# Performance work log

Measured on AMD Instinct MI355X. Metric: run time of the kernel, lower is better.

The kernel has to match this reference:

```python
import jax, jax.numpy as jnp
import numpy as np

B, N, FIN, H, F = 8, 1024, 256, 8, 64
NEG_SLOPE = 0.2


def setup_inputs() -> dict:
    key = jax.random.key(0)
    k = jax.random.split(key, 6)
    x = jax.random.normal(k[0], (B, N, FIN), dtype=jnp.float32)
    adj_mask = jax.random.randint(k[1], (B, N, N), 0, 2, dtype=jnp.int32)
    edge_prior = jax.random.normal(k[2], (B, N, N), dtype=jnp.float32)
    # params (xavier-style scales)
    W = jax.random.normal(k[3], (FIN, H * F), dtype=jnp.float32) * np.sqrt(2.0 / (FIN + H * F))
    a_left = jax.random.normal(k[4], (H, F), dtype=jnp.float32) * np.sqrt(2.0 / (1 + F))
    a_right = jax.random.normal(k[5], (H, F), dtype=jnp.float32) * np.sqrt(2.0 / (1 + F))
    edge_scale = jnp.float32(0.05)
    return {"x": x, "adj_mask": adj_mask, "edge_prior": edge_prior,
            "W": W, "a_left": a_left, "a_right": a_right, "edge_scale": edge_scale}


def reference(x, adj_mask, edge_prior, W, a_left, a_right, edge_scale):
    b, n, _ = x.shape
    h = (x @ W).reshape(b, n, H, F)                      # [B,N,H,F]
    e_left = jnp.einsum('bnhf,hf->bnh', h, a_left)       # [B,N,H]
    e_right = jnp.einsum('bnhf,hf->bnh', h, a_right)     # [B,N,H]
    e = jax.nn.leaky_relu(e_left[:, :, None, :] + e_right[:, None, :, :],
                          negative_slope=NEG_SLOPE)      # [B,N,N,H]
    e = e + edge_scale * edge_prior[..., None]
    e = jnp.where((adj_mask == 0)[..., None], -jnp.inf, e)
    alpha = jax.nn.softmax(e, axis=2)                    # softmax over neighbors j
    h_new = jnp.einsum('bijh,bjhf->bihf', alpha, h)      # [B,N,H,F]
    return h_new.reshape(b, n, H * F)                    # concat=True
```

## Files before the change

### kernel.cpp

```cpp
#include <hip/hip_runtime.h>
#include <hip/hip_bf16.h>

#define B_ 8
#define N_ 1024
#define FIN_ 256
#define H_ 8
#define F_ 64
#define HF_ 512
#define BN_ 8192
#define LOG2E 1.4426950408889634f
#define NEG_ 0.2f

using bf16x8 = __attribute__((ext_vector_type(8))) short;
using f32x4  = __attribute__((ext_vector_type(4))) float;
using i32x4  = __attribute__((ext_vector_type(4))) int;

__device__ __forceinline__ short f2bf(float x) {
  __hip_bfloat16 b = __float2bfloat16(x);
  return *reinterpret_cast<short*>(&b);
}
__device__ __forceinline__ float bf2f(short s) {
  union { unsigned u; float f; } v;
  v.u = ((unsigned)(unsigned short)s) << 16;
  return v.f;
}
__device__ __forceinline__ bf16x8 cvtCE(f32x4 pa, f32x4 pb, i32x4 ma, i32x4 mb, float es) {
  bf16x8 o;
#pragma unroll
  for (int e = 0; e < 4; e++) {
    o[e]     = f2bf(ma[e] != 0 ? es * pa[e] : -1e30f);
    o[e + 4] = f2bf(mb[e] != 0 ? es * pb[e] : -1e30f);
  }
  return o;
}

__global__ __launch_bounds__(256) void k_cvt(
    const float* __restrict__ x, const float* __restrict__ W,
    short* __restrict__ xb, short* __restrict__ Wt) {
  const int bid = blockIdx.x;
  if (bid < 1024) {
    const int idx = (bid * 256 + threadIdx.x) * 8;
    f32x4 a = *(const f32x4*)(x + idx);
    f32x4 b = *(const f32x4*)(x + idx + 4);
    bf16x8 o;
    o[0]=f2bf(a[0]); o[1]=f2bf(a[1]); o[2]=f2bf(a[2]); o[3]=f2bf(a[3]);
    o[4]=f2bf(b[0]); o[5]=f2bf(b[1]); o[6]=f2bf(b[2]); o[7]=f2bf(b[3]);
    *(bf16x8*)(xb + idx) = o;
  } else {
    const int idx = (bid - 1024) * 256 + threadIdx.x;
    const int f = idx >> 8, c = idx & 255;
    Wt[f * FIN_ + c] = f2bf(W[c * HF_ + f]);
  }
}

__global__ __launch_bounds__(256) void k_h(
    const short* __restrict__ Wt, const short* __restrict__ xb,
    const float* __restrict__ aL, const float* __restrict__ aR,
    short* __restrict__ hA, float* __restrict__ el_t, float* __restrict__ er_t) {
  const int nt = blockIdx.x;
  const int h  = blockIdx.y;
  const int w  = threadIdx.x >> 6;
  const int l  = threadIdx.x & 63;
  const int lr = l & 15, lk = l >> 4;
  const int n0 = nt * 64;
  const int fbase = h * 64 + w * 16;

  f32x4 acc[4] = {};
  const short* arow = Wt + (fbase + lr) * FIN_ + lk * 8;

#pragma unroll
  for (int k0 = 0; k0 < FIN_; k0 += 32) {
    bf16x8 a = *(const bf16x8*)(arow + k0);
#pragma unroll
    for (int nf = 0; nf < 4; nf++) {
      bf16x8 bb = *(const bf16x8*)(xb + (size_t)(n0 + nf * 16 + lr) * FIN_ + k0 + lk * 8);
      acc[nf] = __builtin_amdgcn_mfma_f32_16x16x32_bf16(a, bb, acc[nf], 0, 0, 0);
    }
  }

  __shared__ short sT[64][72];
  __shared__ float sEl[4][64], sEr[4][64];
  float al[4], ar[4];
#pragma unroll
  for (int r = 0; r < 4; r++) {
    const int fl = w * 16 + lk * 4 + r;
    al[r] = aL[h * F_ + fl];
    ar[r] = aR[h * F_ + fl];
  }
#pragma unroll
  for (int nf = 0; nf < 4; nf++) {
    const int nl = nf * 16 + lr;
#pragma unroll
    for (int r = 0; r < 4; r++)
      sT[w * 16 + lk * 4 + r][nl] = f2bf(acc[nf][r]);
    float pl = acc[nf][0]*al[0] + acc[nf][1]*al[1] + acc[nf][2]*al[2] + acc[nf][3]*al[3];
    float pr = acc[nf][0]*ar[0] + acc[nf][1]*ar[1] + acc[nf][2]*ar[2] + acc[nf][3]*ar[3];
    pl += __shfl_xor(pl, 16); pl += __shfl_xor(pl, 32);
    pr += __shfl_xor(pr, 16); pr += __shfl_xor(pr, 32);
    if (lk == 0) { sEl[w][nl] = pl; sEr[w][nl] = pr; }
  }
  __syncthreads();
  if (threadIdx.x < 64) {
    const int n = threadIdx.x;
    el_t[h * BN_ + n0 + n] = (sEl[0][n] + sEl[1][n] + sEl[2][n] + sEl[3][n]) * LOG2E;
    er_t[h * BN_ + n0 + n] = (sEr[0][n] + sEr[1][n] + sEr[2][n] + sEr[3][n]) * LOG2E;
  }
  const int b8h = (nt >> 4) * 8 + h;
  const int jb  = (nt & 15) * 2;
#pragma unroll
  for (int gi = 0; gi < 2; gi++) {
    const int g   = threadIdx.x * 2 + gi;
    const int jsl = g >> 8, ff = (g >> 6) & 3, gl = g & 63;
    const int glr = gl & 15, glk = gl >> 4;
    bf16x8 v = *(const bf16x8*)(&sT[ff * 16 + glr][jsl * 32 + glk * 8]);
    *(bf16x8*)(hA + (((size_t)b8h * 32 + jb + jsl) * 4 + ff) * 512 + gl * 8) = v;
  }
}

__global__ __launch_bounds__(512, 2) void k_attn(
    const short* __restrict__ hA, const float* __restrict__ el_t,
    const float* __restrict__ er_t, const float* __restrict__ prior,
    const int* __restrict__ mask, const float* __restrict__ esp,
    float* __restrict__ out) {
  const int bid = blockIdx.x;
  const int b  = bid & 7;
  const int it = bid >> 3;
  const int t  = threadIdx.x;
  const int h  = t >> 6;
  const int l  = t & 63;
  const int lr = l & 15, lk = l >> 4;
  const int i0 = it * 32;
  const size_t bn = (size_t)b * N_;
  const float es = esp[0] * LOG2E;

  __shared__ short cbuf[2][8192];

  const float* elh = el_t + h * BN_ + bn + i0;
  const float el0 = elh[lr], el1 = elh[16 + lr];
  const float* erp = er_t + h * BN_ + bn + lk * 8;
  const short* hW  = hA + (size_t)(b * 8 + h) * 65536 + l * 8;

  const int srow = t >> 4;
  const int c0   = (t & 15) * 2;
  const int sw   = srow & 7;
  const int gA   = (c0 ^ sw) & ~1;
  const int slotA = (srow * 32 + (gA ^ sw)) * 8;
  const int slotB = (srow * 32 + ((gA | 1) ^ sw)) * 8;
  const size_t grow = (bn + i0 + srow) * (size_t)N_;
  const float* pg = prior + grow + gA * 8;
  const int*   mg = mask  + grow + gA * 8;

  {
    f32x4 p0 = *(const f32x4*)(pg),     p1 = *(const f32x4*)(pg + 4);
    f32x4 p2 = *(const f32x4*)(pg + 8), p3 = *(const f32x4*)(pg + 12);
    i32x4 m0 = *(const i32x4*)(mg),     m1 = *(const i32x4*)(mg + 4);
    i32x4 m2 = *(const i32x4*)(mg + 8), m3 = *(const i32x4*)(mg + 12);
    *(bf16x8*)(&cbuf[0][slotA]) = cvtCE(p0, p1, m0, m1, es);
    *(bf16x8*)(&cbuf[0][slotB]) = cvtCE(p2, p3, m2, m3, es);
  }
  bf16x8 hN[4];
#pragma unroll
  for (int ff = 0; ff < 4; ff++) hN[ff] = *(const bf16x8*)(hW + ff * 512);
  __syncthreads();

  f32x4 acc[4][2] = {};
  f32x4 accS[2] = {};
  bf16x8 ones;
#pragma unroll
  for (int e = 0; e < 8; e++) ones[e] = (short)0x3F80;

  for (int ch = 0; ch < 4; ++ch) {
    f32x4 p0, p1, p2, p3; i32x4 m0, m1, m2, m3;
    if (ch < 3) {
      const int off = (ch + 1) * 256;
      p0 = *(const f32x4*)(pg + off);      p1 = *(const f32x4*)(pg + off + 4);
      p2 = *(const f32x4*)(pg + off + 8);  p3 = *(const f32x4*)(pg + off + 12);
      m0 = *(const i32x4*)(mg + off);      m1 = *(const i32x4*)(mg + off + 4);
      m2 = *(const i32x4*)(mg + off + 8);  m3 = *(const i32x4*)(mg + off + 12);
    }
    const short* cb = cbuf[ch & 1];
#pragma unroll
    for (int js = 0; js < 8; ++js) {
      const int s = ch * 8 + js;
      bf16x8 h0 = hN[0], h1 = hN[1], h2 = hN[2], h3 = hN[3];
      const int sn = (s < 31) ? s + 1 : 31;
      const short* hs = hW + (size_t)sn * 2048;
      hN[0] = *(const bf16x8*)(hs);
      hN[1] = *(const bf16x8*)(hs + 512);
      hN[2] = *(const bf16x8*)(hs + 1024);
      hN[3] = *(const bf16x8*)(hs + 1536);
      f32x4 er0 = *(const f32x4*)(erp + s * 32);
      f32x4 er1 = *(const f32x4*)(erp + s * 32 + 4);
      const int ci = ((js * 4 + lk) ^ (lr & 7)) * 8;
      bf16x8 cA = *(const bf16x8*)(cb + lr * 256 + ci);
      bf16x8 cB = *(const bf16x8*)(cb + (16 + lr) * 256 + ci);
      bf16x8 pfA, pfB;
#pragma unroll
      for (int q = 0; q < 4; q++) {
        const float e0 = er0[q], e1 = er1[q];
        float a1 = el0 + e0; a1 = fmaxf(a1, NEG_ * a1); a1 += bf2f(cA[q]);
        float a2 = el0 + e1; a2 = fmaxf(a2, NEG_ * a2); a2 += bf2f(cA[q + 4]);
        float b1 = el1 + e0; b1 = fmaxf(b1, NEG_ * b1); b1 += bf2f(cB[q]);
        float b2 = el1 + e1; b2 = fmaxf(b2, NEG_ * b2); b2 += bf2f(cB[q + 4]);
        float x1, x2, x3, x4;
        asm("v_exp_f32 %0, %1" : "=v"(x1) : "v"(a1));
        asm("v_exp_f32 %0, %1" : "=v"(x2) : "v"(a2));
        asm("v_exp_f32 %0, %1" : "=v"(x3) : "v"(b1));
        asm("v_exp_f32 %0, %1" : "=v"(x4) : "v"(b2));
        pfA[q] = f2bf(x1); pfA[q + 4] = f2bf(x2);
        pfB[q] = f2bf(x3); pfB[q + 4] = f2bf(x4);
      }
      accS[0]   = __builtin_amdgcn_mfma_f32_16x16x32_bf16(ones, pfA, accS[0], 0, 0, 0);
      accS[1]   = __builtin_amdgcn_mfma_f32_16x16x32_bf16(ones, pfB, accS[1], 0, 0, 0);
      acc[0][0] = __builtin_amdgcn_mfma_f32_16x16x32_bf16(h0, pfA, acc[0][0], 0, 0, 0);
      acc[0][1] = __builtin_amdgcn_mfma_f32_16x16x32_bf16(h0, pfB, acc[0][1], 0, 0, 0);
      acc[1][0] = __builtin_amdgcn_mfma_f32_16x16x32_bf16(h1, pfA, acc[1][0], 0, 0, 0);
      acc[1][1] = __builtin_amdgcn_mfma_f32_16x16x32_bf16(h1, pfB, acc[1][1], 0, 0, 0);
      acc[2][0] = __builtin_amdgcn_mfma_f32_16x16x32_bf16(h2, pfA, acc[2][0], 0, 0, 0);
      acc[2][1] = __builtin_amdgcn_mfma_f32_16x16x32_bf16(h2, pfB, acc[2][1], 0, 0, 0);
      acc[3][0] = __builtin_amdgcn_mfma_f32_16x16x32_bf16(h3, pfA, acc[3][0], 0, 0, 0);
      acc[3][1] = __builtin_amdgcn_mfma_f32_16x16x32_bf16(h3, pfB, acc[3][1], 0, 0, 0);
    }
    if (ch < 3) {
      short* nb = (short*)cbuf[(ch + 1) & 1];
      *(bf16x8*)(nb + slotA) = cvtCE(p0, p1, m0, m1, es);
      *(bf16x8*)(nb + slotB) = cvtCE(p2, p3, m2, m3, es);
      __syncthreads();
    }
  }

#pragma unroll
  for (int fi = 0; fi < 2; fi++) {
    const float inv = 1.0f / accS[fi][0];
    const size_t row = bn + i0 + fi * 16 + lr;
#pragma unroll
    for (int ff = 0; ff < 4; ff++) {
      f32x4 v = acc[ff][fi];
      v[0] *= inv; v[1] *= inv; v[2] *= inv; v[3] *= inv;
      *(f32x4*)(out + row * HF_ + h * 64 + ff * 16 + lk * 4) = v;
    }
  }
}

extern "C" void kernel_launch(void* const* d_in, const int* in_sizes, int n_in,
                              void* d_out, int out_size, void* d_ws, size_t ws_size,
                              hipStream_t stream) {
  const float* x     = (const float*)d_in[0];
  const int*   adj   = (const int*)  d_in[1];
  const float* prior = (const float*)d_in[2];
  const float* W     = (const float*)d_in[3];
  const float* aL    = (const float*)d_in[4];
  const float* aR    = (const float*)d_in[5];
  const float* es    = (const float*)d_in[6];
  float* out = (float*)d_out;

  char* ws = (char*)d_ws;
  short* hA   = (short*)ws;
  short* xb   = (short*)(ws + 8u  * 1024 * 1024);
  short* Wt   = (short*)(ws + 12u * 1024 * 1024);
  float* el_t = (float*)(ws + 12u * 1024 * 1024 + 262144);
  float* er_t = (float*)(ws + 12u * 1024 * 1024 + 524288);

  hipLaunchKernelGGL(k_cvt, dim3(1536), dim3(256), 0, stream, x, W, xb, Wt);
  hipLaunchKernelGGL(k_h,   dim3(128, 8), dim3(256), 0, stream,
                     Wt, xb, aL, aR, hA, el_t, er_t);
  hipLaunchKernelGGL(k_attn, dim3(256), dim3(512), 0, stream,
                     hA, el_t, er_t, prior, adj, es, out);
}
```

Baseline: 75.40 us.

## Halve attention row tile to 16, load full prior/mask strip upfront, simplify leaky-relu

The attention kernel now handles 16 query rows per block instead of 32, which doubles the grid to 512 blocks and raises the launch-bounds occupancy hint to 4. The whole 16x1024 prior/mask strip is converted into shared memory once up front, replacing the double-buffered chunk pipeline and its per-chunk barriers. Leaky-ReLU is rewritten as 0.6x+0.4|x| with FMAs. The trade-off is that each hA tile is now read from global memory by twice as many blocks, so the reuse of h across query rows is halved.

```diff
diff --git a/kernel.cpp b/kernel.cpp
--- a/kernel.cpp
+++ b/kernel.cpp
@@ -9,7 +9,6 @@
 #define HF_ 512
 #define BN_ 8192
 #define LOG2E 1.4426950408889634f
-#define NEG_ 0.2f
 
 using bf16x8 = __attribute__((ext_vector_type(8))) short;
 using f32x4  = __attribute__((ext_vector_type(4))) float;
@@ -117,7 +116,7 @@
   }
 }
 
-__global__ __launch_bounds__(512, 2) void k_attn(
+__global__ __launch_bounds__(512, 4) void k_attn(
     const short* __restrict__ hA, const float* __restrict__ el_t,
     const float* __restrict__ er_t, const float* __restrict__ prior,
     const int* __restrict__ mask, const float* __restrict__ esp,
@@ -129,116 +128,88 @@
   const int h  = t >> 6;
   const int l  = t & 63;
   const int lr = l & 15, lk = l >> 4;
-  const int i0 = it * 32;
+  const int i0 = it * 16;
   const size_t bn = (size_t)b * N_;
   const float es = esp[0] * LOG2E;
 
-  __shared__ short cbuf[2][8192];
-
-  const float* elh = el_t + h * BN_ + bn + i0;
-  const float el0 = elh[lr], el1 = elh[16 + lr];
+  __shared__ short cbuf[16 * 1024];
+
+  {
+    const int srow = t >> 5, cg0 = t & 31;
+    const int sw = srow & 7;
+    const size_t grow = (bn + i0 + srow) * (size_t)N_;
+    const float* pg = prior + grow;
+    const int*   mg = mask  + grow;
+#pragma unroll
+    for (int k = 0; k < 4; k++) {
+      const int g = cg0 + 32 * k;
+      f32x4 p0 = *(const f32x4*)(pg + g * 8), p1 = *(const f32x4*)(pg + g * 8 + 4);
+      i32x4 m0 = *(const i32x4*)(mg + g * 8), m1 = *(const i32x4*)(mg + g * 8 + 4);
+      *(bf16x8*)(&cbuf[srow * 1024 + (g ^ sw) * 8]) = cvtCE(p0, p1, m0, m1, es);
+    }
+  }
+
+  const float el = el_t[h * BN_ + bn + i0 + lr];
   const float* erp = er_t + h * BN_ + bn + lk * 8;
   const short* hW  = hA + (size_t)(b * 8 + h) * 65536 + l * 8;
-
-  const int srow = t >> 4;
-  const int c0   = (t & 15) * 2;
-  const int sw   = srow & 7;
-  const int gA   = (c0 ^ sw) & ~1;
-  const int slotA = (srow * 32 + (gA ^ sw)) * 8;
-  const int slotB = (srow * 32 + ((gA | 1) ^ sw)) * 8;
-  const size_t grow = (bn + i0 + srow) * (size_t)N_;
-  const float* pg = prior + grow + gA * 8;
-  const int*   mg = mask  + grow + gA * 8;
-
-  {
-    f32x4 p0 = *(const f32x4*)(pg),     p1 = *(const f32x4*)(pg + 4);
-    f32x4 p2 = *(const f32x4*)(pg + 8), p3 = *(const f32x4*)(pg + 12);
-    i32x4 m0 = *(const i32x4*)(mg),     m1 = *(const i32x4*)(mg + 4);
-    i32x4 m2 = *(const i32x4*)(mg + 8), m3 = *(const i32x4*)(mg + 12);
-    *(bf16x8*)(&cbuf[0][slotA]) = cvtCE(p0, p1, m0, m1, es);
-    *(bf16x8*)(&cbuf[0][slotB]) = cvtCE(p2, p3, m2, m3, es);
-  }
-  bf16x8 hN[4];
-#pragma unroll
-  for (int ff = 0; ff < 4; ff++) hN[ff] = *(const bf16x8*)(hW + ff * 512);
+  const short* cbl = cbuf + lr * 1024;
+  const int xsw = lr & 7;
+
+  bf16x8 hC[4], hN[4];
+#pragma unroll
+  for (int ff = 0; ff < 4; ff++) hC[ff] = *(const bf16x8*)(hW + ff * 512);
+
   __syncthreads();
 
-  f32x4 acc[4][2] = {};
-  f32x4 accS[2] = {};
+  bf16x8 cC = *(const bf16x8*)(cbl + (lk ^ xsw) * 8);
+  f32x4 acc[4] = {};
+  f32x4 accS = {};
   bf16x8 ones;
 #pragma unroll
   for (int e = 0; e < 8; e++) ones[e] = (short)0x3F80;
 
-  for (int ch = 0; ch < 4; ++ch) {
-    f32x4 p0, p1, p2, p3; i32x4 m0, m1, m2, m3;
-    if (ch < 3) {
-      const int off = (ch + 1) * 256;
-      p0 = *(const f32x4*)(pg + off);      p1 = *(const f32x4*)(pg + off + 4);
-      p2 = *(const f32x4*)(pg + off + 8);  p3 = *(const f32x4*)(pg + off + 12);
-      m0 = *(const i32x4*)(mg + off);      m1 = *(const i32x4*)(mg + off + 4);
-      m2 = *(const i32x4*)(mg + off + 8);  m3 = *(const i32x4*)(mg + off + 12);
+  for (int s = 0; s < 32; ++s) {
+    const int sn = (s < 31) ? s + 1 : 31;
+    const short* hs = hW + (size_t)sn * 2048;
+    hN[0] = *(const bf16x8*)(hs);
+    hN[1] = *(const bf16x8*)(hs + 512);
+    hN[2] = *(const bf16x8*)(hs + 1024);
+    hN[3] = *(const bf16x8*)(hs + 1536);
+    bf16x8 cN = *(const bf16x8*)(cbl + (((sn * 4 + lk) ^ xsw) * 8));
+    f32x4 er0 = *(const f32x4*)(erp + s * 32);
+    f32x4 er1 = *(const f32x4*)(erp + s * 32 + 4);
+
+    bf16x8 pf;
+#pragma unroll
+    for (int q = 0; q < 4; q++) {
+      float sA = el + er0[q];
+      float vA = fmaf(0.6f, sA, bf2f(cC[q]));
+      vA = fmaf(0.4f, fabsf(sA), vA);
+      float sB = el + er1[q];
+      float vB = fmaf(0.6f, sB, bf2f(cC[q + 4]));
+      vB = fmaf(0.4f, fabsf(sB), vB);
+      float x1, x2;
+      asm("v_exp_f32 %0, %1" : "=v"(x1) : "v"(vA));
+      asm("v_exp_f32 %0, %1" : "=v"(x2) : "v"(vB));
+      pf[q] = f2bf(x1); pf[q + 4] = f2bf(x2);
     }
-    const short* cb = cbuf[ch & 1];
-#pragma unroll
-    for (int js = 0; js < 8; ++js) {
-      const int s = ch * 8 + js;
-      bf16x8 h0 = hN[0], h1 = hN[1], h2 = hN[2], h3 = hN[3];
-      const int sn = (s < 31) ? s + 1 : 31;
-      const short* hs = hW + (size_t)sn * 2048;
-      hN[0] = *(const bf16x8*)(hs);
-      hN[1] = *(const bf16x8*)(hs + 512);
-      hN[2] = *(const bf16x8*)(hs + 1024);
-      hN[3] = *(const bf16x8*)(hs + 1536);
-      f32x4 er0 = *(const f32x4*)(erp + s * 32);
-      f32x4 er1 = *(const f32x4*)(erp + s * 32 + 4);
-      const int ci = ((js * 4 + lk) ^ (lr & 7)) * 8;
-      bf16x8 cA = *(const bf16x8*)(cb + lr * 256 + ci);
-      bf16x8 cB = *(const bf16x8*)(cb + (16 + lr) * 256 + ci);
-      bf16x8 pfA, pfB;
-#pragma unroll
-      for (int q = 0; q < 4; q++) {
-        const float e0 = er0[q], e1 = er1[q];
-        float a1 = el0 + e0; a1 = fmaxf(a1, NEG_ * a1); a1 += bf2f(cA[q]);
-        float a2 = el0 + e1; a2 = fmaxf(a2, NEG_ * a2); a2 += bf2f(cA[q + 4]);
-        float b1 = el1 + e0; b1 = fmaxf(b1, NEG_ * b1); b1 += bf2f(cB[q]);
-        float b2 = el1 + e1; b2 = fmaxf(b2, NEG_ * b2); b2 += bf2f(cB[q + 4]);
-        float x1, x2, x3, x4;
-        asm("v_exp_f32 %0, %1" : "=v"(x1) : "v"(a1));
-        asm("v_exp_f32 %0, %1" : "=v"(x2) : "v"(a2));
-        asm("v_exp_f32 %0, %1" : "=v"(x3) : "v"(b1));
-        asm("v_exp_f32 %0, %1" : "=v"(x4) : "v"(b2));
-        pfA[q] = f2bf(x1); pfA[q + 4] = f2bf(x2);
-        pfB[q] = f2bf(x3); pfB[q + 4] = f2bf(x4);
-      }
-      accS[0]   = __builtin_amdgcn_mfma_f32_16x16x32_bf16(ones, pfA, accS[0], 0, 0, 0);
-      accS[1]   = __builtin_amdgcn_mfma_f32_16x16x32_bf16(ones, pfB, accS[1], 0, 0, 0);
-      acc[0][0] = __builtin_amdgcn_mfma_f32_16x16x32_bf16(h0, pfA, acc[0][0], 0, 0, 0);
-      acc[0][1] = __builtin_amdgcn_mfma_f32_16x16x32_bf16(h0, pfB, acc[0][1], 0, 0, 0);
-      acc[1][0] = __builtin_amdgcn_mfma_f32_16x16x32_bf16(h1, pfA, acc[1][0], 0, 0, 0);
-      acc[1][1] = __builtin_amdgcn_mfma_f32_16x16x32_bf16(h1, pfB, acc[1][1], 0, 0, 0);
-      acc[2][0] = __builtin_amdgcn_mfma_f32_16x16x32_bf16(h2, pfA, acc[2][0], 0, 0, 0);
-      acc[2][1] = __builtin_amdgcn_mfma_f32_16x16x32_bf16(h2, pfB, acc[2][1], 0, 0, 0);
-      acc[3][0] = __builtin_amdgcn_mfma_f32_16x16x32_bf16(h3, pfA, acc[3][0], 0, 0, 0);
-      acc[3][1] = __builtin_amdgcn_mfma_f32_16x16x32_bf16(h3, pfB, acc[3][1], 0, 0, 0);
-    }
-    if (ch < 3) {
-      short* nb = (short*)cbuf[(ch + 1) & 1];
-      *(bf16x8*)(nb + slotA) = cvtCE(p0, p1, m0, m1, es);
-      *(bf16x8*)(nb + slotB) = cvtCE(p2, p3, m2, m3, es);
-      __syncthreads();
-    }
-  }
-
-#pragma unroll
-  for (int fi = 0; fi < 2; fi++) {
-    const float inv = 1.0f / accS[fi][0];
-    const size_t row = bn + i0 + fi * 16 + lr;
-#pragma unroll
-    for (int ff = 0; ff < 4; ff++) {
-      f32x4 v = acc[ff][fi];
-      v[0] *= inv; v[1] *= inv; v[2] *= inv; v[3] *= inv;
-      *(f32x4*)(out + row * HF_ + h * 64 + ff * 16 + lk * 4) = v;
-    }
+    accS   = __builtin_amdgcn_mfma_f32_16x16x32_bf16(ones, pf, accS, 0, 0, 0);
+    acc[0] = __builtin_amdgcn_mfma_f32_16x16x32_bf16(hC[0], pf, acc[0], 0, 0, 0);
+    acc[1] = __builtin_amdgcn_mfma_f32_16x16x32_bf16(hC[1], pf, acc[1], 0, 0, 0);
+    acc[2] = __builtin_amdgcn_mfma_f32_16x16x32_bf16(hC[2], pf, acc[2], 0, 0, 0);
+    acc[3] = __builtin_amdgcn_mfma_f32_16x16x32_bf16(hC[3], pf, acc[3], 0, 0, 0);
+#pragma unroll
+    for (int ff = 0; ff < 4; ff++) hC[ff] = hN[ff];
+    cC = cN;
+  }
+
+  const float inv = 1.0f / accS[0];
+  const size_t row = bn + i0 + lr;
+#pragma unroll
+  for (int ff = 0; ff < 4; ff++) {
+    f32x4 v = acc[ff];
+    v[0] *= inv; v[1] *= inv; v[2] *= inv; v[3] *= inv;
+    *(f32x4*)(out + row * HF_ + h * 64 + ff * 16 + lk * 4) = v;
   }
 }
 
@@ -264,6 +235,6 @@
   hipLaunchKernelGGL(k_cvt, dim3(1536), dim3(256), 0, stream, x, W, xb, Wt);
   hipLaunchKernelGGL(k_h,   dim3(128, 8), dim3(256), 0, stream,
                      Wt, xb, aL, aR, hA, el_t, er_t);
-  hipLaunchKernelGGL(k_attn, dim3(256), dim3(512), 0, stream,
+  hipLaunchKernelGGL(k_attn, dim3(512), dim3(512), 0, stream,
                      hA, el_t, er_t, prior, adj, es, out);
 }
```

New measurement: 70.74 us. 1.07x faster.
